# Optimization experiments

Measured on AMD Instinct MI355X. Metric: run time of the kernel, lower is better.

## Reference

```python
import jax, jax.numpy as jnp
import numpy as np

B, N, T_OBS, N_HEAD = 64, 512, 8, 4
IN_FEAT = T_OBS * 2          # 16
OUT_FEAT = IN_FEAT * 4       # 64 (GAT out / MLP in)
HID1, HID2 = 1024, 512
S, NSAMP = 2, 20
OUT_DIM = S * NSAMP          # 40


def setup_inputs() -> dict:
    key = jax.random.key(0)
    ks = jax.random.split(key, 12)
    x = jax.random.normal(ks[0], (B, N, T_OBS, 2), dtype=jnp.float32)
    # binary adjacency-style mask over the dense node-node attention
    mask = (jax.random.uniform(ks[1], (B, 1, N, N)) > 0.1).astype(jnp.float32)
    xav = lambda k, shp, fi, fo: jax.random.uniform(k, shp, jnp.float32, -1.0, 1.0) * (1.414 * np.sqrt(6.0 / (fi + fo)))
    w = xav(ks[2], (N_HEAD, IN_FEAT, OUT_FEAT), IN_FEAT, OUT_FEAT)
    a_src = xav(ks[3], (N_HEAD, OUT_FEAT, 1), OUT_FEAT, 1)
    a_dst = xav(ks[4], (N_HEAD, OUT_FEAT, 1), OUT_FEAT, 1)
    bias = jnp.zeros((OUT_FEAT,), jnp.float32)
    lin = lambda k, fi, fo: jax.random.uniform(k, (fi, fo), jnp.float32, -1.0, 1.0) * np.sqrt(1.0 / fi)
    W1 = lin(ks[5], OUT_FEAT, HID1); b1 = jnp.zeros((HID1,), jnp.float32)
    W2 = lin(ks[6], HID1, HID2);     b2 = jnp.zeros((HID2,), jnp.float32)
    W3 = lin(ks[7], HID2, OUT_DIM);  b3 = jnp.zeros((OUT_DIM,), jnp.float32)
    return {"x": x, "mask": mask, "w": w, "a_src": a_src, "a_dst": a_dst,
            "bias": bias, "W1": W1, "b1": b1, "W2": W2, "b2": b2, "W3": W3, "b3": b3}


def reference(x, mask, w, a_src, a_dst, bias, W1, b1, W2, b2, W3, b3):
    b, n = x.shape[0], x.shape[1]
    node = x.reshape(b, n, -1)                                   # [B,N,16]
    # per-head projection: [B,N,16] x [H,16,64] -> [B,H,N,64]
    h_prime = jnp.einsum('bni,hio->bhno', node, w)
    attn_src = jnp.einsum('bhno,ho->bhn', h_prime, a_src[..., 0])
    attn_dst = jnp.einsum('bhno,ho->bhn', h_prime, a_dst[..., 0])
    attn = attn_src[..., :, None] * attn_dst[..., None, :]       # [B,H,N,N] outer product
    attn = jnp.where(attn >= 0, attn, 0.2 * attn)                # leaky_relu(0.2)
    attn = jax.nn.softmax(attn, axis=-1)
    # dropout is identity in eval mode
    attn = attn * mask
    out = jnp.einsum('bhnm,bhmo->bno', attn, h_prime) + bias     # sum over heads fused
    out = out + h_prime.sum(axis=1)                              # skip connection
    # MLP: activation BEFORE each linear (as in original MLP.forward)
    y = out
    for W, bb in ((W1, b1), (W2, b2), (W3, b3)):
        y = jax.nn.relu(y) @ W + bb
    y = y.reshape(b, n, NSAMP, -1)[..., 0:S]                     # [B,N,20,2]
    return jnp.clip(jax.nn.sigmoid(y), 0.01, 0.99)
```

## Files before the change

kernel.cpp:

```cpp
#include <hip/hip_runtime.h>
#include <math.h>

typedef short bf16x8 __attribute__((ext_vector_type(8)));
typedef float f32x4 __attribute__((ext_vector_type(4)));

#define BB 64
#define NN 512
#define NH 4
#define FI 16
#define FO 64
#define HD1 1024
#define HD2 512
#define ODIM 40

__device__ __forceinline__ unsigned short f2bf(float f) {
    unsigned u = __float_as_uint(f);
    u += 0x7fffu + ((u >> 16) & 1u);
    return (unsigned short)(u >> 16);
}
__device__ __forceinline__ unsigned pack2(float a, float b) {
    return (unsigned)f2bf(a) | ((unsigned)f2bf(b) << 16);
}

__global__ void k_wa(const float* __restrict__ w, const float* __restrict__ a_src,
                     const float* __restrict__ a_dst, float* __restrict__ wa)
{
    int t = threadIdx.x;
    int h = t >> 4;
    float s = 0.f, d = 0.f;
    for (int o = 0; o < FO; ++o) {
        float wv = w[t*FO + o];
        s = fmaf(wv, a_src[h*FO + o], s);
        d = fmaf(wv, a_dst[h*FO + o], d);
    }
    wa[t] = s; wa[64 + t] = d;
}

__global__ __launch_bounds__(256) void k_proj2(
    const float* __restrict__ x, const float* __restrict__ w,
    const float* __restrict__ bias, const float* __restrict__ wa,
    short* __restrict__ hpT,
    float* __restrict__ asrc, float* __restrict__ adst,
    float* __restrict__ gat)
{
    __shared__ float xS[64][20];
    __shared__ float gS[NH][64][64];
    int b = blockIdx.y;
    int n0 = blockIdx.x * 64;
    int t = threadIdx.x;
    int h = t >> 6, o = t & 63;
    {
        int n = t >> 2, q = t & 3;
        float4 v = *(const float4*)&x[((size_t)b*NN + n0 + n)*FI + q*4];
        *(float4*)&xS[n][q*4] = v;
    }
    float wreg[16];
#pragma unroll
    for (int i = 0; i < FI; ++i) wreg[i] = w[(h*FI + i)*FO + o];
    __syncthreads();

    short* hb = hpT + (size_t)b * (NH*FO*NN);
    for (int nc = 0; nc < 8; ++nc) {
        float acc[8];
#pragma unroll
        for (int k = 0; k < 8; ++k) {
            int n = nc*8 + k;
            float4 a0 = *(const float4*)&xS[n][0];
            float4 a1 = *(const float4*)&xS[n][4];
            float4 a2 = *(const float4*)&xS[n][8];
            float4 a3 = *(const float4*)&xS[n][12];
            float sA = fmaf(a0.x, wreg[0], fmaf(a0.y, wreg[1], fmaf(a0.z, wreg[2], a0.w*wreg[3])));
            float sB = fmaf(a1.x, wreg[4], fmaf(a1.y, wreg[5], fmaf(a1.z, wreg[6], a1.w*wreg[7])));
            float sC = fmaf(a2.x, wreg[8], fmaf(a2.y, wreg[9], fmaf(a2.z, wreg[10], a2.w*wreg[11])));
            float sD = fmaf(a3.x, wreg[12], fmaf(a3.y, wreg[13], fmaf(a3.z, wreg[14], a3.w*wreg[15])));
            float s = (sA + sB) + (sC + sD);
            acc[k] = s;
            gS[h][n][o] = s;
        }
        uint4 p;
        p.x = pack2(acc[0], acc[1]); p.y = pack2(acc[2], acc[3]);
        p.z = pack2(acc[4], acc[5]); p.w = pack2(acc[6], acc[7]);
        int jt = (n0 >> 5) + (nc >> 2);
        *(uint4*)&hb[(size_t)(jt*256 + h*64 + o)*32 + (nc & 3)*8] = p;
    }
    {
        int n = o;
        float vs = 0.f, vd = 0.f;
#pragma unroll
        for (int i = 0; i < FI; ++i) {
            float xv = xS[n][i];
            vs = fmaf(xv, wa[h*FI + i], vs);
            vd = fmaf(xv, wa[64 + h*FI + i], vd);
        }
        asrc[(size_t)(b*NH + h)*NN + n0 + n] = vs;
        adst[(size_t)(b*NH + h)*NN + n0 + n] = vd;
    }
    __syncthreads();
#pragma unroll
    for (int r = 0; r < 16; ++r) {
        int idx = t + r*256;
        int n = idx >> 6, oo = idx & 63;
        float g = bias[oo] + ((gS[0][n][oo] + gS[1][n][oo]) + (gS[2][n][oo] + gS[3][n][oo]));
        gat[((size_t)b*NN + n0 + n)*FO + oo] = g;
    }
}

__global__ __launch_bounds__(512, 2) void k_attn2(
    const short* __restrict__ hpT, const float* __restrict__ mask,
    const float* __restrict__ asrc, const float* __restrict__ adst,
    float* __restrict__ gat)
{
    __shared__ float dS[NH*NN];
    __shared__ float dmaxS[NH], dminS[NH];
    __shared__ float part[4*4*64*4];
    int b = blockIdx.y;
    int i0blk = blockIdx.x * 64;
    int t = threadIdx.x;
#pragma unroll
    for (int r = 0; r < 4; ++r) {
        int idx = t + r*512;
        dS[idx] = adst[(size_t)b*(NH*NN) + idx];
    }
    __syncthreads();
    int wave = t >> 6, lane = t & 63;
    int wv4 = wave & 3, hh = (wave >> 2) * 2;
    if (wave < 4) {
        float mx = -INFINITY, mn = INFINITY;
        const float* dh = &dS[wave*NN];
#pragma unroll
        for (int q = 0; q < 8; ++q) {
            float v = dh[lane*8 + q];
            mx = fmaxf(mx, v); mn = fminf(mn, v);
        }
#pragma unroll
        for (int off = 1; off < 64; off <<= 1) {
            mx = fmaxf(mx, __shfl_xor(mx, off));
            mn = fminf(mn, __shfl_xor(mn, off));
        }
        if (lane == 0) { dmaxS[wave] = mx; dminS[wave] = mn; }
    }
    __syncthreads();
    int li = lane & 15, kq = lane >> 4;
    int i = i0blk + wv4*16 + li;
    float s[2], m[2], Ssum[2];
#pragma unroll
    for (int h2 = 0; h2 < 2; ++h2) {
        int h = hh + h2;
        s[h2] = asrc[(size_t)(b*NH + h)*NN + i];
        float dm = s[h2] >= 0.f ? dmaxS[h] : dminS[h];
        float l = s[h2] * dm;
        m[h2] = fmaxf(l, 0.2f*l);
        Ssum[h2] = 0.f;
    }
    f32x4 accH[2][4];
#pragma unroll
    for (int h2 = 0; h2 < 2; ++h2)
#pragma unroll
        for (int ot = 0; ot < 4; ++ot) accH[h2][ot] = (f32x4)0.f;

    const float* mrow = &mask[((size_t)b*NN + i)*NN];
    const short* vb = hpT + (size_t)b * (NH*FO*NN);
    float4 mk0 = *(const float4*)&mrow[kq*8];
    float4 mk1 = *(const float4*)&mrow[kq*8 + 4];
    for (int jt = 0; jt < 16; ++jt) {
        float4 c0 = mk0, c1 = mk1;
        if (jt < 15) {
            mk0 = *(const float4*)&mrow[(jt+1)*32 + kq*8];
            mk1 = *(const float4*)&mrow[(jt+1)*32 + kq*8 + 4];
        }
        int j0 = jt*32;
        float mk[8] = {c0.x, c0.y, c0.z, c0.w, c1.x, c1.y, c1.z, c1.w};
#pragma unroll
        for (int h2 = 0; h2 < 2; ++h2) {
            int h = hh + h2;
            float4 d0 = *(const float4*)&dS[h*NN + j0 + kq*8];
            float4 d1 = *(const float4*)&dS[h*NN + j0 + kq*8 + 4];
            float dv[8] = {d0.x,d0.y,d0.z,d0.w,d1.x,d1.y,d1.z,d1.w};
            float u[8];
#pragma unroll
            for (int q = 0; q < 8; ++q) {
                float v = s[h2]*dv[q];
                v = fmaxf(v, 0.2f*v);
                u[q] = __expf(v - m[h2]);
            }
            Ssum[h2] += ((u[0]+u[1]) + (u[2]+u[3])) + ((u[4]+u[5]) + (u[6]+u[7]));
            union { bf16x8 v; unsigned uu[4]; } pf;
#pragma unroll
            for (int q = 0; q < 4; ++q)
                pf.uu[q] = pack2(u[2*q]*mk[2*q], u[2*q+1]*mk[2*q+1]);
#pragma unroll
            for (int ot = 0; ot < 4; ++ot) {
                bf16x8 vf = *(const bf16x8*)&vb[(size_t)(jt*256 + h*64 + ot*16 + li)*32 + kq*8];
                accH[h2][ot] = __builtin_amdgcn_mfma_f32_16x16x32_bf16(pf.v, vf, accH[h2][ot], 0, 0, 0);
            }
        }
    }
#pragma unroll
    for (int h2 = 0; h2 < 2; ++h2) {
        Ssum[h2] += __shfl_xor(Ssum[h2], 16);
        Ssum[h2] += __shfl_xor(Ssum[h2], 32);
    }
    float rinv[2][4];
#pragma unroll
    for (int h2 = 0; h2 < 2; ++h2)
#pragma unroll
        for (int g = 0; g < 4; ++g)
            rinv[h2][g] = 1.0f / __shfl(Ssum[h2], kq*4 + g);
    f32x4 contrib[4];
#pragma unroll
    for (int ot = 0; ot < 4; ++ot)
#pragma unroll
        for (int g = 0; g < 4; ++g)
            contrib[ot][g] = accH[0][ot][g]*rinv[0][g] + accH[1][ot][g]*rinv[1][g];
    if (wave < 4) {
#pragma unroll
        for (int ot = 0; ot < 4; ++ot) {
            float4 v = {contrib[ot][0], contrib[ot][1], contrib[ot][2], contrib[ot][3]};
            *(float4*)&part[((wv4*4 + ot)*64 + lane)*4] = v;
        }
    }
    __syncthreads();
    if (wave >= 4) {
#pragma unroll
        for (int ot = 0; ot < 4; ++ot) {
            float4 p = *(const float4*)&part[((wv4*4 + ot)*64 + lane)*4];
#pragma unroll
            for (int g = 0; g < 4; ++g) {
                int ii = i0blk + wv4*16 + kq*4 + g;
                int oo = ot*16 + li;
                size_t ix = ((size_t)b*NN + ii)*FO + oo;
                float pg = (g == 0) ? p.x : (g == 1) ? p.y : (g == 2) ? p.z : p.w;
                gat[ix] += contrib[ot][g] + pg;
            }
        }
    }
}

__global__ __launch_bounds__(256) void k_conv(
    const float* __restrict__ W1, const float* __restrict__ W2, const float* __restrict__ W3,
    short* __restrict__ w1t, short* __restrict__ w2f, short* __restrict__ w3t)
{
    int idx = blockIdx.x * 256 + threadIdx.x;
    if (idx < HD1*FO) {
        int n = idx >> 6, k = idx & 63;
        w1t[idx] = (short)f2bf(W1[k*HD1 + n]);
    } else if (idx < HD1*FO + HD2*HD1) {
        int i2 = idx - HD1*FO;
        int e = i2 & 7, kqq = (i2 >> 3) & 3, n = (i2 >> 5) & 511, ks = i2 >> 14;
        int k = ks*32 + kqq*8 + e;
        w2f[i2] = (short)f2bf(W2[k*HD2 + n]);
    } else if (idx < HD1*FO + HD2*HD1 + 48*HD2) {
        int i3 = idx - (HD1*FO + HD2*HD1);
        int n = i3 >> 9, k = i3 & 511;
        w3t[i3] = (short)(n < ODIM ? f2bf(W3[k*ODIM + n]) : 0);
    }
}

__global__ __launch_bounds__(256, 2) void k_mlpA(
    const float* __restrict__ gat,
    const short* __restrict__ w1t, const float* __restrict__ b1,
    short* __restrict__ h1f)
{
    __shared__ char a0b[8192];
    int t = threadIdx.x;
    int lane = t & 63, wave = t >> 6;
    int li = lane & 15, kq = lane >> 4;
    int m0 = blockIdx.x * 64;

    {
        int row = t >> 2, c0 = (t & 3) * 16;
        const float4* g = (const float4*)&gat[(size_t)(m0 + row) * FO + c0];
        float4 v0 = g[0], v1 = g[1], v2 = g[2], v3 = g[3];
        uint4 p0, p1;
        p0.x = pack2(fmaxf(v0.x,0.f), fmaxf(v0.y,0.f));
        p0.y = pack2(fmaxf(v0.z,0.f), fmaxf(v0.w,0.f));
        p0.z = pack2(fmaxf(v1.x,0.f), fmaxf(v1.y,0.f));
        p0.w = pack2(fmaxf(v1.z,0.f), fmaxf(v1.w,0.f));
        p1.x = pack2(fmaxf(v2.x,0.f), fmaxf(v2.y,0.f));
        p1.y = pack2(fmaxf(v2.z,0.f), fmaxf(v2.w,0.f));
        p1.z = pack2(fmaxf(v3.x,0.f), fmaxf(v3.y,0.f));
        p1.w = pack2(fmaxf(v3.z,0.f), fmaxf(v3.w,0.f));
        int base = row*128 + c0*2;
        *(uint4*)(a0b + (base ^ ((row&7)<<4)))      = p0;
        *(uint4*)(a0b + ((base+16) ^ ((row&7)<<4))) = p1;
    }
    __syncthreads();

    for (int c = 0; c < 4; ++c) {
        int n0 = wave * 256 + c * 64;
        f32x4 acc[4][4];
#pragma unroll
        for (int mt = 0; mt < 4; ++mt)
#pragma unroll
            for (int nt = 0; nt < 4; ++nt) acc[mt][nt] = (f32x4)0.f;
#pragma unroll
        for (int ks = 0; ks < 2; ++ks) {
            int k0 = ks * 32;
            bf16x8 xf[4];
#pragma unroll
            for (int mt = 0; mt < 4; ++mt) {
                int row = mt * 16 + li;
                int addr = (row * 128 + k0 * 2 + kq * 16) ^ ((row & 7) << 4);
                xf[mt] = *(bf16x8*)(a0b + addr);
            }
#pragma unroll
            for (int nt = 0; nt < 4; ++nt) {
                int col = n0 + nt * 16 + li;
                bf16x8 wf = *(const bf16x8*)(w1t + col * 64 + k0 + kq * 8);
#pragma unroll
                for (int mt = 0; mt < 4; ++mt)
                    acc[mt][nt] = __builtin_amdgcn_mfma_f32_16x16x32_bf16(wf, xf[mt], acc[mt][nt], 0, 0, 0);
            }
        }
#pragma unroll
        for (int mt = 0; mt < 4; ++mt)
#pragma unroll
            for (int nt = 0; nt < 4; ++nt) {
                int m = mt * 16 + li;
                int nb = n0 + nt * 16 + kq * 4;
                float4 bb = *(const float4*)&b1[nb];
                float v0 = fmaxf(acc[mt][nt][0] + bb.x, 0.f);
                float v1 = fmaxf(acc[mt][nt][1] + bb.y, 0.f);
                float v2 = fmaxf(acc[mt][nt][2] + bb.z, 0.f);
                float v3 = fmaxf(acc[mt][nt][3] + bb.w, 0.f);
                uint2 pw; pw.x = pack2(v0, v1); pw.y = pack2(v2, v3);
                int ks2 = wave*8 + c*2 + (nt >> 1);
                int kq2 = ((nt*2) + (kq >> 1)) & 3;
                int e0  = (kq & 1) * 4;
                size_t dst = (size_t)ks2*1048576 + (size_t)(m0 + m)*32 + kq2*8 + e0;
                *(uint2*)&h1f[dst] = pw;
            }
    }
}

__global__ __launch_bounds__(512, 2) void k_mlpB(
    const short* __restrict__ h1f,
    const short* __restrict__ w2f, const float* __restrict__ b2,
    const short* __restrict__ w3t, const float* __restrict__ b3,
    float* __restrict__ out)
{
    extern __shared__ char smem[];
    int t = threadIdx.x;
    int lane = t & 63, wave = t >> 6;
    int li = lane & 15, kq = lane >> 4;
    int m0 = blockIdx.x * 128;

    const short* xbase = h1f + (size_t)(m0 + li) * 32 + kq * 8;
    const short* wbase = w2f + ((size_t)(wave*64 + li)*4 + kq)*8;

    f32x4 acc2[8][4];
#pragma unroll
    for (int mt = 0; mt < 8; ++mt)
#pragma unroll
        for (int nt = 0; nt < 4; ++nt) acc2[mt][nt] = (f32x4)0.f;

    bf16x8 xf[2][8], wf[2][4];
#define LOADI(P, KS) do { \
    _Pragma("unroll") \
    for (int mt_ = 0; mt_ < 8; ++mt_) \
        xf[P][mt_] = *(const bf16x8*)(xbase + (size_t)(KS)*1048576 + mt_*512); \
    _Pragma("unroll") \
    for (int nt_ = 0; nt_ < 4; ++nt_) \
        wf[P][nt_] = *(const bf16x8*)(wbase + (size_t)(KS)*16384 + nt_*512); \
} while (0)

    LOADI(0, 0);
    LOADI(1, 1);
#pragma unroll 2
    for (int ks = 0; ks < 32; ++ks) {
        int p = ks & 1;
#pragma unroll
        for (int nt = 0; nt < 4; ++nt)
#pragma unroll
            for (int mt = 0; mt < 8; ++mt)
                acc2[mt][nt] = __builtin_amdgcn_mfma_f32_16x16x32_bf16(wf[p][nt], xf[p][mt], acc2[mt][nt], 0, 0, 0);
        if (ks < 30) LOADI(p, ks + 2);
    }
#undef LOADI

#pragma unroll
    for (int mt = 0; mt < 8; ++mt)
#pragma unroll
        for (int nt = 0; nt < 4; ++nt) {
            int m = mt * 16 + li;
            int nb = wave * 64 + nt * 16 + kq * 4;
            float4 bb = *(const float4*)&b2[nb];
            float v0 = fmaxf(acc2[mt][nt][0] + bb.x, 0.f);
            float v1 = fmaxf(acc2[mt][nt][1] + bb.y, 0.f);
            float v2 = fmaxf(acc2[mt][nt][2] + bb.z, 0.f);
            float v3 = fmaxf(acc2[mt][nt][3] + bb.w, 0.f);
            uint2 pw; pw.x = pack2(v0, v1); pw.y = pack2(v2, v3);
            int addr = (m * 1024 + nb * 2) ^ ((m & 7) << 4);
            *(uint2*)(smem + addr) = pw;
        }
    __syncthreads();

    f32x4 acc3[3];
#pragma unroll
    for (int nt = 0; nt < 3; ++nt) acc3[nt] = (f32x4)0.f;
#pragma unroll
    for (int ks = 0; ks < 16; ++ks) {
        int k0 = ks * 32;
        int m = wave * 16 + li;
        int addr = (m * 1024 + k0 * 2 + kq * 16) ^ ((m & 7) << 4);
        bf16x8 xfr = *(bf16x8*)(smem + addr);
#pragma unroll
        for (int nt = 0; nt < 3; ++nt) {
            int col = nt * 16 + li;
            bf16x8 wfr = *(const bf16x8*)(w3t + col * 512 + k0 + kq * 8);
            acc3[nt] = __builtin_amdgcn_mfma_f32_16x16x32_bf16(wfr, xfr, acc3[nt], 0, 0, 0);
        }
    }
#pragma unroll
    for (int nt = 0; nt < 3; ++nt)
#pragma unroll
        for (int g = 0; g < 4; ++g) {
            int n = nt * 16 + kq * 4 + g;
            if (n < ODIM) {
                int m = wave * 16 + li;
                float s = acc3[nt][g] + b3[n];
                s = 1.f / (1.f + __expf(-s));
                s = fminf(fmaxf(s, 0.01f), 0.99f);
                out[(size_t)(m0 + m) * ODIM + n] = s;
            }
        }
}

extern "C" void kernel_launch(void* const* d_in, const int* in_sizes, int n_in,
                              void* d_out, int out_size, void* d_ws, size_t ws_size,
                              hipStream_t stream)
{
    const float* x     = (const float*)d_in[0];
    const float* mask  = (const float*)d_in[1];
    const float* w     = (const float*)d_in[2];
    const float* a_src = (const float*)d_in[3];
    const float* a_dst = (const float*)d_in[4];
    const float* bias  = (const float*)d_in[5];
    const float* W1    = (const float*)d_in[6];
    const float* b1    = (const float*)d_in[7];
    const float* W2    = (const float*)d_in[8];
    const float* b2    = (const float*)d_in[9];
    const float* W3    = (const float*)d_in[10];
    const float* b3    = (const float*)d_in[11];
    float* out = (float*)d_out;

    char* p = (char*)d_ws;
    short* h1f = (short*)p;
    short* hpT = (short*)p;  p += (size_t)BB*NH*FO*NN*2;
    float* asrc = (float*)p; p += (size_t)BB*NH*NN*4;
    float* adst = (float*)p; p += (size_t)BB*NH*NN*4;
    p = (char*)d_ws + (size_t)BB*NN*HD1*2;
    float* gat  = (float*)p; p += (size_t)BB*NN*FO*4;
    short* w1t  = (short*)p; p += (size_t)HD1*FO*2;
    short* w2f  = (short*)p; p += (size_t)HD2*HD1*2;
    short* w3t  = (short*)p; p += (size_t)48*HD2*2;
    float* wa   = (float*)p; p += 128*4;

    k_wa   <<<1, 64, 0, stream>>>(w, a_src, a_dst, wa);
    k_conv <<<(HD1*FO + HD2*HD1 + 48*HD2)/256, 256, 0, stream>>>(W1, W2, W3, w1t, w2f, w3t);
    k_proj2<<<dim3(NN/64, BB), 256, 0, stream>>>(x, w, bias, wa, hpT, asrc, adst, gat);
    k_attn2<<<dim3(NN/64, BB), 512, 0, stream>>>(hpT, mask, asrc, adst, gat);
    k_mlpA <<<BB*NN/64, 256, 0, stream>>>(gat, w1t, b1, h1f);
    k_mlpB <<<BB*NN/128, 512, 131072, stream>>>(h1f, w2f, b2, w3t, b3, out);
}
```

Before: 167.4 us.

## Split MLP layer-2 hidden dim across blocks with atomic partial layer-3 sums

The second MLP kernel now splits the 512-wide hidden dimension into four 128-column slices, each handled by its own 256-thread block. This gives four times as many blocks, a much smaller shared-memory footprint (32KB instead of 128KB) and higher occupancy. Each block computes a partial layer-3 product over its slice and atomically adds it into a float accumulator, which the projection kernel zeroes. A new small kernel then applies bias, sigmoid and clamp. Blocks are also remapped in an XCD-aware order, and the explicit double-buffered register prefetch is dropped. The costs are extra atomics, one more launch, and the h1 activations being re-read by four blocks each.

After: 276.5 us. +65.2%, slower.

```diff
diff --git a/kernel.cpp b/kernel.cpp
--- a/kernel.cpp
+++ b/kernel.cpp
@@ -41,7 +41,7 @@
     const float* __restrict__ bias, const float* __restrict__ wa,
     short* __restrict__ hpT,
     float* __restrict__ asrc, float* __restrict__ adst,
-    float* __restrict__ gat)
+    float* __restrict__ gat, float* __restrict__ pacc)
 {
     __shared__ float xS[64][20];
     __shared__ float gS[NH][64][64];
@@ -49,6 +49,11 @@
     int n0 = blockIdx.x * 64;
     int t = threadIdx.x;
     int h = t >> 6, o = t & 63;
+    {
+        size_t base = (size_t)(b*NN + n0) * ODIM;
+#pragma unroll
+        for (int r = 0; r < 10; ++r) pacc[base + t + r*256] = 0.f;
+    }
     {
         int n = t >> 2, q = t & 3;
         float4 v = *(const float4*)&x[((size_t)b*NN + n0 + n)*FI + q*4];
@@ -333,97 +338,110 @@
     }
 }
 
-__global__ __launch_bounds__(512, 2) void k_mlpB(
+__global__ __launch_bounds__(256, 3) void k_mlpB(
     const short* __restrict__ h1f,
     const short* __restrict__ w2f, const float* __restrict__ b2,
-    const short* __restrict__ w3t, const float* __restrict__ b3,
-    float* __restrict__ out)
-{
-    extern __shared__ char smem[];
+    const short* __restrict__ w3t, float* __restrict__ pacc)
+{
+    __shared__ char h2q[32768];
     int t = threadIdx.x;
     int lane = t & 63, wave = t >> 6;
     int li = lane & 15, kq = lane >> 4;
-    int m0 = blockIdx.x * 128;
+    int swz = blockIdx.x;
+    int xcd = swz & 7, rest = swz >> 3;
+    int mtile = xcd + 8 * (rest >> 2);
+    int nh = rest & 3;
+    int m0 = mtile * 128;
 
     const short* xbase = h1f + (size_t)(m0 + li) * 32 + kq * 8;
-    const short* wbase = w2f + ((size_t)(wave*64 + li)*4 + kq)*8;
-
-    f32x4 acc2[8][4];
+    const short* wbase = w2f + ((size_t)(nh*128 + wave*32 + li) * 4 + kq) * 8;
+
+    f32x4 acc2[8][2];
 #pragma unroll
     for (int mt = 0; mt < 8; ++mt)
 #pragma unroll
-        for (int nt = 0; nt < 4; ++nt) acc2[mt][nt] = (f32x4)0.f;
-
-    bf16x8 xf[2][8], wf[2][4];
-#define LOADI(P, KS) do { \
-    _Pragma("unroll") \
-    for (int mt_ = 0; mt_ < 8; ++mt_) \
-        xf[P][mt_] = *(const bf16x8*)(xbase + (size_t)(KS)*1048576 + mt_*512); \
-    _Pragma("unroll") \
-    for (int nt_ = 0; nt_ < 4; ++nt_) \
-        wf[P][nt_] = *(const bf16x8*)(wbase + (size_t)(KS)*16384 + nt_*512); \
-} while (0)
-
-    LOADI(0, 0);
-    LOADI(1, 1);
-#pragma unroll 2
+        for (int nt = 0; nt < 2; ++nt) acc2[mt][nt] = (f32x4)0.f;
+
     for (int ks = 0; ks < 32; ++ks) {
-        int p = ks & 1;
-#pragma unroll
-        for (int nt = 0; nt < 4; ++nt)
+        bf16x8 xf[8], wf[2];
+#pragma unroll
+        for (int mt = 0; mt < 8; ++mt)
+            xf[mt] = *(const bf16x8*)(xbase + (size_t)ks*1048576 + mt*512);
+#pragma unroll
+        for (int nt = 0; nt < 2; ++nt)
+            wf[nt] = *(const bf16x8*)(wbase + (size_t)ks*16384 + nt*512);
+#pragma unroll
+        for (int nt = 0; nt < 2; ++nt)
 #pragma unroll
             for (int mt = 0; mt < 8; ++mt)
-                acc2[mt][nt] = __builtin_amdgcn_mfma_f32_16x16x32_bf16(wf[p][nt], xf[p][mt], acc2[mt][nt], 0, 0, 0);
-        if (ks < 30) LOADI(p, ks + 2);
-    }
-#undef LOADI
+                acc2[mt][nt] = __builtin_amdgcn_mfma_f32_16x16x32_bf16(wf[nt], xf[mt], acc2[mt][nt], 0, 0, 0);
+    }
 
 #pragma unroll
     for (int mt = 0; mt < 8; ++mt)
 #pragma unroll
-        for (int nt = 0; nt < 4; ++nt) {
+        for (int nt = 0; nt < 2; ++nt) {
             int m = mt * 16 + li;
-            int nb = wave * 64 + nt * 16 + kq * 4;
-            float4 bb = *(const float4*)&b2[nb];
+            int nl = wave*32 + nt*16 + kq*4;
+            int n = nh*128 + nl;
+            float4 bb = *(const float4*)&b2[n];
             float v0 = fmaxf(acc2[mt][nt][0] + bb.x, 0.f);
             float v1 = fmaxf(acc2[mt][nt][1] + bb.y, 0.f);
             float v2 = fmaxf(acc2[mt][nt][2] + bb.z, 0.f);
             float v3 = fmaxf(acc2[mt][nt][3] + bb.w, 0.f);
             uint2 pw; pw.x = pack2(v0, v1); pw.y = pack2(v2, v3);
-            int addr = (m * 1024 + nb * 2) ^ ((m & 7) << 4);
-            *(uint2*)(smem + addr) = pw;
-        }
-    __syncthreads();
-
-    f32x4 acc3[3];
-#pragma unroll
-    for (int nt = 0; nt < 3; ++nt) acc3[nt] = (f32x4)0.f;
-#pragma unroll
-    for (int ks = 0; ks < 16; ++ks) {
+            int addr = (m * 256 + nl * 2) ^ ((m & 7) << 4);
+            *(uint2*)(h2q + addr) = pw;
+        }
+    __syncthreads();
+
+    f32x4 acc3[2][3];
+#pragma unroll
+    for (int hf = 0; hf < 2; ++hf)
+#pragma unroll
+        for (int nt = 0; nt < 3; ++nt) acc3[hf][nt] = (f32x4)0.f;
+#pragma unroll
+    for (int ks = 0; ks < 4; ++ks) {
         int k0 = ks * 32;
-        int m = wave * 16 + li;
-        int addr = (m * 1024 + k0 * 2 + kq * 16) ^ ((m & 7) << 4);
-        bf16x8 xfr = *(bf16x8*)(smem + addr);
+        bf16x8 xf2[2];
+#pragma unroll
+        for (int hf = 0; hf < 2; ++hf) {
+            int m = wave*32 + hf*16 + li;
+            int addr = (m * 256 + k0 * 2 + kq * 16) ^ ((m & 7) << 4);
+            xf2[hf] = *(bf16x8*)(h2q + addr);
+        }
 #pragma unroll
         for (int nt = 0; nt < 3; ++nt) {
             int col = nt * 16 + li;
-            bf16x8 wfr = *(const bf16x8*)(w3t + col * 512 + k0 + kq * 8);
-            acc3[nt] = __builtin_amdgcn_mfma_f32_16x16x32_bf16(wfr, xfr, acc3[nt], 0, 0, 0);
-        }
-    }
-#pragma unroll
-    for (int nt = 0; nt < 3; ++nt)
-#pragma unroll
-        for (int g = 0; g < 4; ++g) {
-            int n = nt * 16 + kq * 4 + g;
-            if (n < ODIM) {
-                int m = wave * 16 + li;
-                float s = acc3[nt][g] + b3[n];
-                s = 1.f / (1.f + __expf(-s));
-                s = fminf(fmaxf(s, 0.01f), 0.99f);
-                out[(size_t)(m0 + m) * ODIM + n] = s;
-            }
-        }
+            bf16x8 wf = *(const bf16x8*)(w3t + col * 512 + nh*128 + k0 + kq * 8);
+#pragma unroll
+            for (int hf = 0; hf < 2; ++hf)
+                acc3[hf][nt] = __builtin_amdgcn_mfma_f32_16x16x32_bf16(wf, xf2[hf], acc3[hf][nt], 0, 0, 0);
+        }
+    }
+#pragma unroll
+    for (int hf = 0; hf < 2; ++hf)
+#pragma unroll
+        for (int nt = 0; nt < 3; ++nt)
+#pragma unroll
+            for (int g = 0; g < 4; ++g) {
+                int n = nt * 16 + kq * 4 + g;
+                if (n < ODIM) {
+                    int m = m0 + wave*32 + hf*16 + li;
+                    atomicAdd(&pacc[(size_t)m * ODIM + n], acc3[hf][nt][g]);
+                }
+            }
+}
+
+__global__ __launch_bounds__(256) void k_sig(
+    const float* __restrict__ pacc, const float* __restrict__ b3, float* __restrict__ out)
+{
+    int idx = blockIdx.x * 256 + threadIdx.x;
+    int mm = idx / ODIM, n = idx - mm * ODIM;
+    float s = pacc[idx] + b3[n];
+    s = 1.f / (1.f + __expf(-s));
+    s = fminf(fmaxf(s, 0.01f), 0.99f);
+    out[idx] = s;
 }
 
 extern "C" void kernel_launch(void* const* d_in, const int* in_sizes, int n_in,
@@ -455,11 +473,13 @@
     short* w2f  = (short*)p; p += (size_t)HD2*HD1*2;
     short* w3t  = (short*)p; p += (size_t)48*HD2*2;
     float* wa   = (float*)p; p += 128*4;
+    float* pacc = (float*)p; p += (size_t)BB*NN*ODIM*4;
 
     k_wa   <<<1, 64, 0, stream>>>(w, a_src, a_dst, wa);
     k_conv <<<(HD1*FO + HD2*HD1 + 48*HD2)/256, 256, 0, stream>>>(W1, W2, W3, w1t, w2f, w3t);
-    k_proj2<<<dim3(NN/64, BB), 256, 0, stream>>>(x, w, bias, wa, hpT, asrc, adst, gat);
+    k_proj2<<<dim3(NN/64, BB), 256, 0, stream>>>(x, w, bias, wa, hpT, asrc, adst, gat, pacc);
     k_attn2<<<dim3(NN/64, BB), 512, 0, stream>>>(hpT, mask, asrc, adst, gat);
     k_mlpA <<<BB*NN/64, 256, 0, stream>>>(gat, w1t, b1, h1f);
-    k_mlpB <<<BB*NN/128, 512, 131072, stream>>>(h1f, w2f, b2, w3t, b3, out);
-}
+    k_mlpB <<<BB*NN/128*4, 256, 0, stream>>>(h1f, w2f, b2, w3t, pacc);
+    k_sig  <<<BB*NN*ODIM/256, 256, 0, stream>>>(pacc, b3, out);
+}
```
